# Performance work log

Hardware: AMD Instinct MI355X
Metric: run time of the kernel (lower is better)

Reference implementation:

```python
import jax, jax.numpy as jnp
import numpy as np

D_MODEL = 1024
N_HEADS = 16
THETA = 10000.0


def _rope(x, token_positions):
    # x: (b, h, s, d_k); token_positions: (b, s)
    d_k = x.shape[-1]
    powers = jnp.arange(0, d_k, 2, dtype=jnp.float32) / d_k        # (d_k/2,)
    freqs = 1.0 / (THETA ** powers)
    ang = token_positions.astype(jnp.float32)[..., None] * freqs   # (b, s, d_k/2)
    cos = jnp.cos(ang)[:, None, :, :].astype(x.dtype)              # (b, 1, s, d_k/2)
    sin = jnp.sin(ang)[:, None, :, :].astype(x.dtype)
    x_even = x[..., ::2]
    x_odd = x[..., 1::2]
    r1 = x_even * cos - x_odd * sin
    r2 = x_even * sin + x_odd * cos
    # interleave back to (..., d_k)
    return jnp.stack([r1, r2], axis=-1).reshape(x.shape)


def reference(x, token_positions, wq, wk, wv, wo):
    B, S, D = x.shape
    H = N_HEADS
    d_k = D // H

    def proj(w):
        y = jnp.einsum('bsi,oi->bso', x, w)
        return y.reshape(B, S, H, d_k).transpose(0, 2, 1, 3)  # (b, h, s, d_k)

    q = _rope(proj(wq), token_positions)
    k = _rope(proj(wk), token_positions)
    v = proj(wv)

    scale = 1.0 / jnp.sqrt(jnp.asarray(d_k, dtype=x.dtype))
    score = jnp.einsum('bhqd,bhkd->bhqk', q, k) * scale  # (b, h, s, s)
    causal = jnp.tril(jnp.ones((S, S), dtype=bool))
    score = jnp.where(causal, score, -jnp.inf)
    probs = jax.nn.softmax(score, axis=-1)
    attn = jnp.einsum('bhqk,bhkd->bhqd', probs, v)
    attn = attn.transpose(0, 2, 1, 3).reshape(B, S, D)
    return jnp.einsum('bsi,oi->bso', attn, wo)


def setup_inputs() -> dict:
    key = jax.random.key(0)
    ks = jax.random.split(key, 6)
    B, S, D = 2, 2048, D_MODEL
    std = (2.0 / (D + D)) ** 0.5
    x = jax.random.normal(ks[0], (B, S, D), dtype=jnp.float32)
    token_positions = jnp.broadcast_to(jnp.arange(S, dtype=jnp.int32), (B, S))
    wq = jax.random.normal(ks[1], (D, D), dtype=jnp.float32) * std
    wk = jax.random.normal(ks[2], (D, D), dtype=jnp.float32) * std
    wv = jax.random.normal(ks[3], (D, D), dtype=jnp.float32) * std
    wo = jax.random.normal(ks[4], (D, D), dtype=jnp.float32) * std
    return {"x": x, "token_positions": token_positions, "wq": wq, "wk": wk, "wv": wv, "wo": wo}
```

## Files before the change

### kernel.cpp

```cpp
#include <hip/hip_runtime.h>
#include <hip/hip_bf16.h>

typedef unsigned short u16;
typedef unsigned int u32;
typedef short short8 __attribute__((ext_vector_type(8)));
typedef u16 u16x8 __attribute__((ext_vector_type(8)));
typedef u16 u16x4 __attribute__((ext_vector_type(4)));
typedef u32 u32x4 __attribute__((ext_vector_type(4)));
typedef float f32x4 __attribute__((ext_vector_type(4)));
typedef float f32x16 __attribute__((ext_vector_type(16)));

#define MFMA(a, b, c) __builtin_amdgcn_mfma_f32_16x16x32_bf16((a), (b), (c), 0, 0, 0)
#define MFMA32(a, b, c) __builtin_amdgcn_mfma_f32_32x32x16_bf16((a), (b), (c), 0, 0, 0)

#define QSCALE 0.18033688011112042f

__device__ __forceinline__ u16 f2bf(float f) {
  unsigned u = __float_as_uint(f);
  unsigned r = (u + 0x7fffu + ((u >> 16) & 1u)) >> 16;
  return (u16)r;
}
__device__ __forceinline__ float bf2f(u16 h) {
  return __uint_as_float(((unsigned)h) << 16);
}
__device__ __forceinline__ float exp2hw(float x) {
  float r;
  asm("v_exp_f32 %0, %1" : "=v"(r) : "v"(x));
  return r;
}
__device__ __forceinline__ u32 cvtpk(float lo, float hi) {
  u32 d;
  asm("v_cvt_pk_bf16_f32 %0, %1, %2" : "=v"(d) : "v"(lo), "v"(hi));
  return d;
}
__device__ __forceinline__ void plswap(u32& a, u32& b) {
  asm volatile("v_permlane32_swap_b32 %0, %1" : "+v"(a), "+v"(b));
}
__device__ __forceinline__ void async16(const void* g, void* l) {
  __builtin_amdgcn_global_load_lds(
      (const __attribute__((address_space(1))) void*)g,
      (__attribute__((address_space(3))) void*)l, 16, 0, 0);
}
__device__ __forceinline__ f32x16 zero16() {
  f32x16 z;
#pragma unroll
  for (int i = 0; i < 16; i++) z[i] = 0.f;
  return z;
}
#define WAITV(N) asm volatile("s_waitcnt vmcnt(" #N ")" ::: "memory")
#define WAITL0() asm volatile("s_waitcnt lgkmcnt(0)" ::: "memory")
#define BAR() __builtin_amdgcn_s_barrier()
#define PRIO1 __builtin_amdgcn_s_setprio(1)
#define PRIO0 __builtin_amdgcn_s_setprio(0)

__global__ __launch_bounds__(256) void convert_kernel(
    const float* __restrict__ x, const float* __restrict__ wq,
    const float* __restrict__ wk, const float* __restrict__ wv,
    const float* __restrict__ wo, u16* __restrict__ ws) {
  int blk = blockIdx.x;
  const float* src; u16* dst;
  if (blk < 2048)      { src = x;  dst = ws; }
  else if (blk < 2560) { src = wq; dst = ws + 4194304;               blk -= 2048; }
  else if (blk < 3072) { src = wk; dst = ws + 4194304 + 1048576;     blk -= 2560; }
  else if (blk < 3584) { src = wv; dst = ws + 4194304 + 2 * 1048576; blk -= 3072; }
  else                 { src = wo; dst = ws + 4194304 + 3 * 1048576; blk -= 3584; }
  int idx = (blk * 256 + threadIdx.x) * 8;
  float4 v0 = *(const float4*)(src + idx);
  float4 v1 = *(const float4*)(src + idx + 4);
  u16x8 o;
  o[0] = f2bf(v0.x); o[1] = f2bf(v0.y); o[2] = f2bf(v0.z); o[3] = f2bf(v0.w);
  o[4] = f2bf(v1.x); o[5] = f2bf(v1.y); o[6] = f2bf(v1.z); o[7] = f2bf(v1.w);
  *(u16x8*)(dst + idx) = o;
}

__global__ __launch_bounds__(256) void rope_table(const int* __restrict__ tp,
                                                  float* __restrict__ tab) {
  int t = blockIdx.x * 256 + threadIdx.x;
  int bs = t >> 5, p = t & 31;
  float freq = exp2hw(-(float)p * 0.4152410118609203f);
  float ang = (float)tp[bs] * freq;
  float sn, cs;
  sincosf(ang, &sn, &cs);
  tab[bs * 64 + p * 2] = cs;
  tab[bs * 64 + p * 2 + 1] = sn;
}

__global__ __launch_bounds__(512, 2) void gemm_qkv256(
    const u16* __restrict__ xb, const u16* __restrict__ Wg,
    const float* __restrict__ tab, u16* __restrict__ qb, u16* __restrict__ kb,
    u16* __restrict__ vt) {
  __shared__ u16 As[2][16384];
  __shared__ u16 Bs[2][12288];
  const int tid = threadIdx.x, lane = tid & 63, wid = tid >> 6;
  const int wm = wid >> 2, wn = wid & 3;
  const int g = lane >> 4, r = lane & 15;
  const int rowBase = blockIdx.y << 8;
  const int colBase = blockIdx.x * 192;

#define STG_A(BUF, T)                                                         \
  do {                                                                        \
    _Pragma("unroll") for (int i_ = 0; i_ < 4; ++i_) {                        \
      int c = i_ * 512 + tid;                                                 \
      int row = c >> 3, kc = ((c & 7) ^ (row & 7)) * 8;                       \
      async16(xb + (size_t)(rowBase + row) * 1024 + (T)*64 + kc,              \
              (char*)As[BUF] + c * 16);                                       \
    }                                                                         \
  } while (0)
#define STG_B(BUF, T)                                                         \
  do {                                                                        \
    _Pragma("unroll") for (int i_ = 0; i_ < 3; ++i_) {                        \
      int c = i_ * 512 + tid;                                                 \
      int row = c >> 3, kc = ((c & 7) ^ (row & 7)) * 8;                       \
      async16(Wg + (size_t)(colBase + row) * 1024 + (T)*64 + kc,              \
              (char*)Bs[BUF] + c * 16);                                       \
    }                                                                         \
  } while (0)

  f32x4 acc[8][3];
#pragma unroll
  for (int m = 0; m < 8; m++)
#pragma unroll
    for (int n = 0; n < 3; n++) acc[m][n] = (f32x4){0.f, 0.f, 0.f, 0.f};
  short8 af[4][2], bfr[3][2];

#define RD_A(CUR, MH)                                                         \
  do {                                                                        \
    _Pragma("unroll") for (int mi = 0; mi < 4; mi++) {                        \
      int ra = wm * 128 + (MH)*64 + mi * 16 + r;                              \
      const u16* p = As[CUR] + ra * 64;                                       \
      int sw = (ra & 7) << 3;                                                 \
      af[mi][0] = *(const short8*)(p + ((g << 3) ^ sw));                      \
      af[mi][1] = *(const short8*)(p + (((4 + g) << 3) ^ sw));                \
    }                                                                         \
  } while (0)
#define RD_B(CUR)                                                             \
  do {                                                                        \
    _Pragma("unroll") for (int ni = 0; ni < 3; ni++) {                        \
      int cb = wn * 48 + ni * 16 + r;                                         \
      const u16* p = Bs[CUR] + cb * 64;                                       \
      int sw = (cb & 7) << 3;                                                 \
      bfr[ni][0] = *(const short8*)(p + ((g << 3) ^ sw));                     \
      bfr[ni][1] = *(const short8*)(p + (((4 + g) << 3) ^ sw));               \
    }                                                                         \
  } while (0)
#define MM24(MH)                                                              \
  do {                                                                        \
    _Pragma("unroll") for (int mi = 0; mi < 4; mi++)                          \
        _Pragma("unroll") for (int ni = 0; ni < 3; ni++) {                    \
      acc[(MH)*4 + mi][ni] = MFMA(af[mi][0], bfr[ni][0], acc[(MH)*4 + mi][ni]); \
      acc[(MH)*4 + mi][ni] = MFMA(af[mi][1], bfr[ni][1], acc[(MH)*4 + mi][ni]); \
    }                                                                         \
  } while (0)

  STG_A(0, 0); STG_B(0, 0);
  STG_A(1, 1);
  WAITV(4);
  BAR();

  for (int t = 0; t < 16; ++t) {
    const int cur = t & 1, nxt = cur ^ 1;
    RD_A(cur, 0);
    RD_B(cur);
    if (t < 15) STG_B(nxt, t + 1);
    BAR(); WAITL0();
    PRIO1; MM24(0); PRIO0; BAR();
    RD_A(cur, 1);
    if (t < 14) {
      STG_A(cur, t + 2);
      WAITV(4);
    } else {
      WAITV(0);
    }
    BAR(); WAITL0();
    PRIO1; MM24(1); PRIO0; BAR();
  }
#undef STG_A
#undef STG_B
#undef RD_A
#undef RD_B
#undef MM24

  const int colF = colBase + wn * 48;
#pragma unroll
  for (int n = 0; n < 3; n++) {
    const int col3 = colF + n * 16 + r;
    const int z = col3 >> 10;
    const int col = col3 & 1023;
    if (z < 2) {
      u16* dst = z ? kb : qb;
      const float qs = z ? 1.0f : QSCALE;
      const int p2 = (col >> 1) & 31;
      const bool odd = col & 1;
#pragma unroll
      for (int m = 0; m < 8; m++)
#pragma unroll
        for (int i = 0; i < 4; i++) {
          const int row = rowBase + wm * 128 + m * 16 + g * 4 + i;
          float2 cssn = *(const float2*)(tab + row * 64 + p2 * 2);
          float v = acc[m][n][i];
          float part = __shfl_xor(v, 1);
          float res = odd ? (part * cssn.y + v * cssn.x)
                          : (v * cssn.x - part * cssn.y);
          dst[(size_t)row * 1024 + col] = f2bf(res * qs);
        }
    } else {
#pragma unroll
      for (int m = 0; m < 8; m++)
#pragma unroll
        for (int i = 0; i < 4; i++) {
          const int row = rowBase + wm * 128 + m * 16 + g * 4 + i;
          const int bb = row >> 11, s = row & 2047;
          vt[(size_t)((bb * 16 + (col >> 6)) * 64 + (col & 63)) * 2048 + s] =
              f2bf(acc[m][n][i]);
        }
    }
  }
}

__device__ __forceinline__ void gemm_tile(const u16* __restrict__ A,
                                          const u16* __restrict__ Bm, int K,
                                          int rowBase, int colBase, u16* As,
                                          u16* Bs, f32x4 acc[4][4]) {
  const int tid = threadIdx.x;
  const int lane = tid & 63, wid = tid >> 6;
  const int wr = wid >> 1, wc = wid & 1;
  const int g = lane >> 4, r = lane & 15;

#pragma unroll
  for (int m = 0; m < 4; m++)
#pragma unroll
    for (int n = 0; n < 4; n++) acc[m][n] = (f32x4){0.f, 0.f, 0.f, 0.f};

#define GSTAGE(KT, BUF)                                                       \
  do {                                                                        \
    _Pragma("unroll") for (int i_ = 0; i_ < 4; ++i_) {                        \
      int c = i_ * 256 + tid;                                                 \
      int row = c >> 3, kc = (c & 7) ^ (row & 7);                             \
      async16(A + (size_t)(rowBase + row) * K + ((KT) << 6) + kc * 8,         \
              (char*)As + (BUF)*16384 + c * 16);                              \
    }                                                                         \
    _Pragma("unroll") for (int i_ = 0; i_ < 4; ++i_) {                        \
      int c = i_ * 256 + tid;                                                 \
      int row = c >> 3, kc = (c & 7) ^ (row & 7);                             \
      async16(Bm + (size_t)(colBase + row) * K + ((KT) << 6) + kc * 8,        \
              (char*)Bs + (BUF)*16384 + c * 16);                              \
    }                                                                         \
  } while (0)

  const int nkt = K >> 6;
  GSTAGE(0, 0);
  for (int kt = 0; kt < nkt; ++kt) {
    const int cur = kt & 1;
    if (kt + 1 < nkt) {
      GSTAGE(kt + 1, cur ^ 1);
      WAITV(8);
    } else {
      WAITV(0);
    }
    BAR();
    const u16* Ab = As + cur * 8192;
    const u16* Bb = Bs + cur * 8192;
#pragma unroll
    for (int ks = 0; ks < 2; ++ks) {
      short8 af[4], bfr[4];
#pragma unroll
      for (int m = 0; m < 4; m++) {
        int rr = wr * 64 + m * 16 + r;
        af[m] = *(const short8*)(Ab + rr * 64 + (((ks * 4 + g) ^ (rr & 7)) << 3));
      }
#pragma unroll
      for (int n = 0; n < 4; n++) {
        int rr = wc * 64 + n * 16 + r;
        bfr[n] = *(const short8*)(Bb + rr * 64 + (((ks * 4 + g) ^ (rr & 7)) << 3));
      }
#pragma unroll
      for (int m = 0; m < 4; m++)
#pragma unroll
        for (int n = 0; n < 4; n++)
          acc[m][n] = MFMA(af[m], bfr[n], acc[m][n]);
    }
    WAITL0();
    BAR();
  }
#undef GSTAGE
}

__global__ __launch_bounds__(256, 4) void attn_kernel(
    const u16* __restrict__ qg, const u16* __restrict__ kg,
    const u16* __restrict__ vt, u16* __restrict__ p0, u16* __restrict__ p1,
    float* __restrict__ mbuf, float* __restrict__ lbuf) {
  __shared__ u16 Ks[2][64 * 64];
  __shared__ u16 Vs[2][64 * 64];
  const int tid = threadIdx.x, wid = tid >> 6, lane = tid & 63;
  const int q5 = lane & 31, hi = lane >> 5;
  const int akc = blockIdx.x >> 5, bh = blockIdx.x & 31;
  const int a = akc >> 2, k = (akc >> 1) & 1, c = akc & 1;
  const int b = bh >> 4, h = bh & 15;
  const int base = (wid < 2) ? a : (15 - a);
  const int rb = base * 128 + k * 64 + (wid & 1) * 32;
  const int cmax = rb >> 5;
  const int jend = 30 - 2 * a + k;
  const int qrow = (b << 11) + rb + q5;

  short8 bq[4];
  {
    const u16* qp = qg + (size_t)qrow * 1024 + (h << 6) + hi * 8;
    bq[0] = *(const short8*)(qp);
    bq[1] = *(const short8*)(qp + 16);
    bq[2] = *(const short8*)(qp + 32);
    bq[3] = *(const short8*)(qp + 48);
  }
  f32x16 accO0 = zero16(), accO1 = zero16();
  float m_r = -1e30f, l_r = 0.f;

#define STAGE(JT, BUF)                                                        \
  do {                                                                        \
    _Pragma("unroll") for (int i_ = 0; i_ < 2; i_++) {                        \
      int cc_ = i_ * 256 + tid;                                               \
      int row = cc_ >> 3, cc = (cc_ & 7) ^ (row & 7);                         \
      async16(kg + (size_t)((b << 11) + ((JT) << 6) + row) * 1024 +           \
                  (h << 6) + cc * 8,                                          \
              (char*)Ks[BUF] + cc_ * 16);                                     \
      async16(vt + (size_t)((bh << 6) + row) * 2048 + ((JT) << 6) + cc * 8,   \
              (char*)Vs[BUF] + cc_ * 16);                                     \
    }                                                                         \
  } while (0)

  if (c <= jend) STAGE(c, 0);

  for (int jj = c; jj <= jend; jj += 2) {
    const int cur = ((jj - c) >> 1) & 1;
    if (jj + 2 <= jend) {
      STAGE(jj + 2, cur ^ 1);
      WAITV(4);
    } else {
      WAITV(0);
    }
    BAR();
    if (2 * jj <= cmax) {
      const u16* Kb = Ks[cur];
      const u16* Vb = Vs[cur];
      const bool has1 = (2 * jj + 1 <= cmax);
      const int rsw = (q5 & 7) << 3;
      f32x16 s0 = zero16(), s1 = zero16();
      PRIO1;
#pragma unroll
      for (int kk = 0; kk < 4; kk++) {
        short8 kf =
            *(const short8*)(Kb + q5 * 64 + ((((kk << 1) + hi) << 3) ^ rsw));
        s0 = MFMA32(kf, bq[kk], s0);
      }
      PRIO0;
      if (has1) {
        PRIO1;
#pragma unroll
        for (int kk = 0; kk < 4; kk++) {
          short8 kf = *(const short8*)(Kb + (32 + q5) * 64 +
                                       ((((kk << 1) + hi) << 3) ^ rsw));
          s1 = MFMA32(kf, bq[kk], s1);
        }
        PRIO0;
      }
      if (2 * jj == cmax) {
#pragma unroll
        for (int rg = 0; rg < 16; rg++) {
          int rowk = (rg & 3) + 8 * (rg >> 2) + 4 * hi;
          if (rowk > q5) s0[rg] = -1e30f;
        }
      } else if (2 * jj + 1 == cmax) {
#pragma unroll
        for (int rg = 0; rg < 16; rg++) {
          int rowk = (rg & 3) + 8 * (rg >> 2) + 4 * hi;
          if (rowk > q5) s1[rg] = -1e30f;
        }
      }
      float pmax = s0[0];
#pragma unroll
      for (int rg = 1; rg < 16; rg++) pmax = fmaxf(pmax, s0[rg]);
      if (has1) {
#pragma unroll
        for (int rg = 0; rg < 16; rg++) pmax = fmaxf(pmax, s1[rg]);
      }
      pmax = fmaxf(pmax, __shfl_xor(pmax, 32));
      if (!__all(pmax <= m_r + 8.0f)) {
        float mn = fmaxf(m_r, pmax);
        float sc = exp2hw(m_r - mn);
        l_r *= sc;
#pragma unroll
        for (int rg = 0; rg < 16; rg++) {
          accO0[rg] *= sc;
          accO1[rg] *= sc;
        }
        m_r = mn;
      }
      float rs = 0.f;
      u32 pw00[4], pw01[4], pw10[4], pw11[4];
#define PACK(SREG, OUT, S16)                                                  \
  do {                                                                        \
    float pp0 = exp2hw(SREG[(S16)*8 + 0] - m_r);                              \
    float pp1 = exp2hw(SREG[(S16)*8 + 1] - m_r);                              \
    float pp2 = exp2hw(SREG[(S16)*8 + 2] - m_r);                              \
    float pp3 = exp2hw(SREG[(S16)*8 + 3] - m_r);                              \
    float pp4 = exp2hw(SREG[(S16)*8 + 4] - m_r);                              \
    float pp5 = exp2hw(SREG[(S16)*8 + 5] - m_r);                              \
    float pp6 = exp2hw(SREG[(S16)*8 + 6] - m_r);                              \
    float pp7 = exp2hw(SREG[(S16)*8 + 7] - m_r);                              \
    rs += ((pp0 + pp1) + (pp2 + pp3)) + ((pp4 + pp5) + (pp6 + pp7));          \
    u32 X = cvtpk(pp0, pp1), Y = cvtpk(pp2, pp3);                             \
    u32 U = cvtpk(pp4, pp5), W = cvtpk(pp6, pp7);                             \
    plswap(X, U);                                                             \
    plswap(Y, W);                                                             \
    OUT[0] = X; OUT[1] = Y; OUT[2] = U; OUT[3] = W;                           \
  } while (0)
      PACK(s0, pw00, 0);
      PACK(s0, pw01, 1);
      if (has1) {
        PACK(s1, pw10, 0);
        PACK(s1, pw11, 1);
      }
#undef PACK
      rs += __shfl_xor(rs, 32);
      l_r += rs;
#define PVSTEP(PW, CH)                                                        \
  do {                                                                        \
    u32x4 pv_ = {PW[0], PW[1], PW[2], PW[3]};                                 \
    short8 pb_ = __builtin_bit_cast(short8, pv_);                             \
    short8 v0_ =                                                              \
        *(const short8*)(Vb + q5 * 64 + ((((CH) + hi) << 3) ^ rsw));          \
    short8 v1_ = *(const short8*)(Vb + (32 + q5) * 64 +                       \
                                  ((((CH) + hi) << 3) ^ rsw));                \
    accO0 = MFMA32(v0_, pb_, accO0);                                          \
    accO1 = MFMA32(v1_, pb_, accO1);                                          \
  } while (0)
      PRIO1;
      PVSTEP(pw00, 0);
      PVSTEP(pw01, 2);
      if (has1) {
        PVSTEP(pw10, 4);
        PVSTEP(pw11, 6);
      }
      PRIO0;
#undef PVSTEP
    }
    WAITL0();
    BAR();
  }
#undef STAGE

  u16* pout = c ? p1 : p0;
#pragma unroll
  for (int qd = 0; qd < 4; qd++) {
    u16x4 o0, o1;
#pragma unroll
    for (int e = 0; e < 4; e++) {
      o0[e] = f2bf(accO0[qd * 4 + e]);
      o1[e] = f2bf(accO1[qd * 4 + e]);
    }
    u16* op = pout + (size_t)qrow * 1024 + (h << 6) + qd * 8 + hi * 4;
    *(u16x4*)(op) = o0;
    *(u16x4*)(op + 32) = o1;
  }
  if (hi == 0) {
    int mli = c * 65536 + (bh << 11) + rb + q5;
    mbuf[mli] = m_r;
    lbuf[mli] = l_r;
  }
}

__global__ __launch_bounds__(256) void attn_merge(const u16* __restrict__ p1,
                                                  const float* __restrict__ mbuf,
                                                  const float* __restrict__ lbuf,
                                                  u16* __restrict__ ab) {
  int t = blockIdx.x * 256 + threadIdx.x;
  int dg = t & 7, row = t >> 3;
  int bh = row >> 11, s = row & 2047;
  int b = bh >> 4, h = bh & 15;
  size_t addr = (size_t)((b << 11) + s) * 1024 + (h << 6) + dg * 8;
  float m0 = mbuf[row], m1 = mbuf[65536 + row];
  float l0 = lbuf[row], l1 = lbuf[65536 + row];
  float m = fmaxf(m0, m1);
  float w0 = exp2hw(m0 - m), w1 = exp2hw(m1 - m);
  float inv = 1.0f / (l0 * w0 + l1 * w1);
  u16x8 o0 = *(const u16x8*)(ab + addr);
  u16x8 o1 = *(const u16x8*)(p1 + addr);
  u16x8 o;
#pragma unroll
  for (int i = 0; i < 8; i++)
    o[i] = f2bf((bf2f(o0[i]) * w0 + bf2f(o1[i]) * w1) * inv);
  *(u16x8*)(ab + addr) = o;
}

__global__ __launch_bounds__(256) void gemm_ao(const u16* __restrict__ ab,
                                               const u16* __restrict__ wob,
                                               float* __restrict__ out) {
  __shared__ u16 As[2][128 * 64], Bs[2][128 * 64];
  f32x4 acc[4][4];
  gemm_tile(ab, wob, 1024, blockIdx.y * 128, blockIdx.x * 128, As[0], Bs[0], acc);
  const int lane = threadIdx.x & 63, wid = threadIdx.x >> 6;
  const int wr = wid >> 1, wc = wid & 1, g = lane >> 4, r = lane & 15;
  const int rowB = blockIdx.y * 128 + wr * 64;
  const int colB = blockIdx.x * 128 + wc * 64;
#pragma unroll
  for (int m = 0; m < 4; m++)
#pragma unroll
    for (int n = 0; n < 4; n++)
#pragma unroll
      for (int i = 0; i < 4; i++)
        out[(size_t)(rowB + m * 16 + g * 4 + i) * 1024 + colB + n * 16 + r] =
            acc[m][n][i];
}

extern "C" void kernel_launch(void* const* d_in, const int* in_sizes, int n_in,
                              void* d_out, int out_size, void* d_ws,
                              size_t ws_size, hipStream_t stream) {
  const float* x = (const float*)d_in[0];
  const int* tp = (const int*)d_in[1];
  const float* wq = (const float*)d_in[2];
  const float* wk = (const float*)d_in[3];
  const float* wv = (const float*)d_in[4];
  const float* wo = (const float*)d_in[5];
  float* out = (float*)d_out;

  u16* ws = (u16*)d_ws;
  u16* xb = ws;
  u16* wqb = xb + 4194304;
  u16* wkb = wqb + 1048576;
  u16* wvb = wkb + 1048576;
  u16* wob = wvb + 1048576;
  u16* qb = wob + 1048576;
  u16* kb = qb + 4194304;
  u16* vtb = kb + 4194304;
  u16* ab = vtb + 4194304;
  float* tab = (float*)ab;
  float* mbuf = (float*)wqb;
  float* lbuf = (float*)wkb;

  convert_kernel<<<4096, 256, 0, stream>>>(x, wq, wk, wv, wo, ws);
  rope_table<<<512, 256, 0, stream>>>(tp, tab);
  gemm_qkv256<<<dim3(16, 16), 512, 0, stream>>>(xb, wqb, tab, qb, kb, vtb);
  attn_kernel<<<1024, 256, 0, stream>>>(qb, kb, vtb, ab, xb, mbuf, lbuf);
  attn_merge<<<2048, 256, 0, stream>>>(xb, mbuf, lbuf, ab);
  gemm_ao<<<dim3(8, 32), 256, 0, stream>>>(ab, wob, out);
}
```

Measured before the change: 115.5 us.

## Split attention KV range four ways with single-buffer LDS and fuse rope table

Attention now splits each query block's key range into four interleaved chunks instead of two, doubling the grid to 2048 blocks. It drops LDS double buffering to single buffers and raises the launch-bounds occupancy target from 4 to 7. The merge kernel combines four partials, and the rope table generation is folded into the convert kernel to save a launch. The intent is more parallelism and occupancy, at the cost of losing load/compute overlap within a block, extra partial-output traffic, and more merge work.

```diff
diff --git a/kernel.cpp b/kernel.cpp
--- a/kernel.cpp
+++ b/kernel.cpp
@@ -56,8 +56,20 @@
 __global__ __launch_bounds__(256) void convert_kernel(
     const float* __restrict__ x, const float* __restrict__ wq,
     const float* __restrict__ wk, const float* __restrict__ wv,
-    const float* __restrict__ wo, u16* __restrict__ ws) {
+    const float* __restrict__ wo, u16* __restrict__ ws,
+    const int* __restrict__ tp, float* __restrict__ tab) {
   int blk = blockIdx.x;
+  if (blk >= 4096) {
+    int t = (blk - 4096) * 256 + threadIdx.x;
+    int bs = t >> 5, p = t & 31;
+    float freq = exp2hw(-(float)p * 0.4152410118609203f);
+    float ang = (float)tp[bs] * freq;
+    float sn, cs;
+    sincosf(ang, &sn, &cs);
+    tab[bs * 64 + p * 2] = cs;
+    tab[bs * 64 + p * 2 + 1] = sn;
+    return;
+  }
   const float* src; u16* dst;
   if (blk < 2048)      { src = x;  dst = ws; }
   else if (blk < 2560) { src = wq; dst = ws + 4194304;               blk -= 2048; }
@@ -71,18 +83,6 @@
   o[0] = f2bf(v0.x); o[1] = f2bf(v0.y); o[2] = f2bf(v0.z); o[3] = f2bf(v0.w);
   o[4] = f2bf(v1.x); o[5] = f2bf(v1.y); o[6] = f2bf(v1.z); o[7] = f2bf(v1.w);
   *(u16x8*)(dst + idx) = o;
-}
-
-__global__ __launch_bounds__(256) void rope_table(const int* __restrict__ tp,
-                                                  float* __restrict__ tab) {
-  int t = blockIdx.x * 256 + threadIdx.x;
-  int bs = t >> 5, p = t & 31;
-  float freq = exp2hw(-(float)p * 0.4152410118609203f);
-  float ang = (float)tp[bs] * freq;
-  float sn, cs;
-  sincosf(ang, &sn, &cs);
-  tab[bs * 64 + p * 2] = cs;
-  tab[bs * 64 + p * 2 + 1] = sn;
 }
 
 __global__ __launch_bounds__(512, 2) void gemm_qkv256(
@@ -285,16 +285,17 @@
 #undef GSTAGE
 }
 
-__global__ __launch_bounds__(256, 4) void attn_kernel(
+__global__ __launch_bounds__(256, 7) void attn_kernel(
     const u16* __restrict__ qg, const u16* __restrict__ kg,
     const u16* __restrict__ vt, u16* __restrict__ p0, u16* __restrict__ p1,
-    float* __restrict__ mbuf, float* __restrict__ lbuf) {
-  __shared__ u16 Ks[2][64 * 64];
-  __shared__ u16 Vs[2][64 * 64];
+    u16* __restrict__ p2, u16* __restrict__ p3, float* __restrict__ mbuf,
+    float* __restrict__ lbuf) {
+  __shared__ u16 Ks[64 * 64];
+  __shared__ u16 Vs[64 * 64];
   const int tid = threadIdx.x, wid = tid >> 6, lane = tid & 63;
   const int q5 = lane & 31, hi = lane >> 5;
   const int akc = blockIdx.x >> 5, bh = blockIdx.x & 31;
-  const int a = akc >> 2, k = (akc >> 1) & 1, c = akc & 1;
+  const int a = akc >> 3, k = (akc >> 2) & 1, c = akc & 3;
   const int b = bh >> 4, h = bh & 15;
   const int base = (wid < 2) ? a : (15 - a);
   const int rb = base * 128 + k * 64 + (wid & 1) * 32;
@@ -313,33 +314,25 @@
   f32x16 accO0 = zero16(), accO1 = zero16();
   float m_r = -1e30f, l_r = 0.f;
 
-#define STAGE(JT, BUF)                                                        \
+#define STAGE(JT)                                                             \
   do {                                                                        \
     _Pragma("unroll") for (int i_ = 0; i_ < 2; i_++) {                        \
       int cc_ = i_ * 256 + tid;                                               \
       int row = cc_ >> 3, cc = (cc_ & 7) ^ (row & 7);                         \
       async16(kg + (size_t)((b << 11) + ((JT) << 6) + row) * 1024 +           \
                   (h << 6) + cc * 8,                                          \
-              (char*)Ks[BUF] + cc_ * 16);                                     \
+              (char*)Ks + cc_ * 16);                                          \
       async16(vt + (size_t)((bh << 6) + row) * 2048 + ((JT) << 6) + cc * 8,   \
-              (char*)Vs[BUF] + cc_ * 16);                                     \
-    }                                                                         \
-  } while (0)
-
-  if (c <= jend) STAGE(c, 0);
-
-  for (int jj = c; jj <= jend; jj += 2) {
-    const int cur = ((jj - c) >> 1) & 1;
-    if (jj + 2 <= jend) {
-      STAGE(jj + 2, cur ^ 1);
-      WAITV(4);
-    } else {
-      WAITV(0);
-    }
+              (char*)Vs + cc_ * 16);                                          \
+    }                                                                         \
+  } while (0)
+
+  STAGE(c);
+
+  for (int jj = c; jj <= jend; jj += 4) {
+    WAITV(0);
     BAR();
     if (2 * jj <= cmax) {
-      const u16* Kb = Ks[cur];
-      const u16* Vb = Vs[cur];
       const bool has1 = (2 * jj + 1 <= cmax);
       const int rsw = (q5 & 7) << 3;
       f32x16 s0 = zero16(), s1 = zero16();
@@ -347,7 +340,7 @@
 #pragma unroll
       for (int kk = 0; kk < 4; kk++) {
         short8 kf =
-            *(const short8*)(Kb + q5 * 64 + ((((kk << 1) + hi) << 3) ^ rsw));
+            *(const short8*)(Ks + q5 * 64 + ((((kk << 1) + hi) << 3) ^ rsw));
         s0 = MFMA32(kf, bq[kk], s0);
       }
       PRIO0;
@@ -355,7 +348,7 @@
         PRIO1;
 #pragma unroll
         for (int kk = 0; kk < 4; kk++) {
-          short8 kf = *(const short8*)(Kb + (32 + q5) * 64 +
+          short8 kf = *(const short8*)(Ks + (32 + q5) * 64 +
                                        ((((kk << 1) + hi) << 3) ^ rsw));
           s1 = MFMA32(kf, bq[kk], s1);
         }
@@ -426,8 +419,8 @@
     u32x4 pv_ = {PW[0], PW[1], PW[2], PW[3]};                                 \
     short8 pb_ = __builtin_bit_cast(short8, pv_);                             \
     short8 v0_ =                                                              \
-        *(const short8*)(Vb + q5 * 64 + ((((CH) + hi) << 3) ^ rsw));          \
-    short8 v1_ = *(const short8*)(Vb + (32 + q5) * 64 +                       \
+        *(const short8*)(Vs + q5 * 64 + ((((CH) + hi) << 3) ^ rsw));          \
+    short8 v1_ = *(const short8*)(Vs + (32 + q5) * 64 +                       \
                                   ((((CH) + hi) << 3) ^ rsw));                \
     accO0 = MFMA32(v0_, pb_, accO0);                                          \
     accO1 = MFMA32(v1_, pb_, accO1);                                          \
@@ -444,10 +437,11 @@
     }
     WAITL0();
     BAR();
+    if (jj + 4 <= jend) STAGE(jj + 4);
   }
 #undef STAGE
 
-  u16* pout = c ? p1 : p0;
+  u16* pout = (c == 0) ? p0 : (c == 1) ? p1 : (c == 2) ? p2 : p3;
 #pragma unroll
   for (int qd = 0; qd < 4; qd++) {
     u16x4 o0, o1;
@@ -467,26 +461,33 @@
   }
 }
 
-__global__ __launch_bounds__(256) void attn_merge(const u16* __restrict__ p1,
-                                                  const float* __restrict__ mbuf,
-                                                  const float* __restrict__ lbuf,
-                                                  u16* __restrict__ ab) {
+__global__ __launch_bounds__(256) void attn_merge(
+    const u16* __restrict__ p1, const u16* __restrict__ p2,
+    const u16* __restrict__ p3, const float* __restrict__ mbuf,
+    const float* __restrict__ lbuf, u16* __restrict__ ab) {
   int t = blockIdx.x * 256 + threadIdx.x;
   int dg = t & 7, row = t >> 3;
   int bh = row >> 11, s = row & 2047;
   int b = bh >> 4, h = bh & 15;
   size_t addr = (size_t)((b << 11) + s) * 1024 + (h << 6) + dg * 8;
   float m0 = mbuf[row], m1 = mbuf[65536 + row];
+  float m2 = mbuf[131072 + row], m3 = mbuf[196608 + row];
   float l0 = lbuf[row], l1 = lbuf[65536 + row];
-  float m = fmaxf(m0, m1);
+  float l2 = lbuf[131072 + row], l3 = lbuf[196608 + row];
+  float m = fmaxf(fmaxf(m0, m1), fmaxf(m2, m3));
   float w0 = exp2hw(m0 - m), w1 = exp2hw(m1 - m);
-  float inv = 1.0f / (l0 * w0 + l1 * w1);
+  float w2 = exp2hw(m2 - m), w3 = exp2hw(m3 - m);
+  float inv = 1.0f / (l0 * w0 + l1 * w1 + l2 * w2 + l3 * w3);
   u16x8 o0 = *(const u16x8*)(ab + addr);
   u16x8 o1 = *(const u16x8*)(p1 + addr);
+  u16x8 o2 = *(const u16x8*)(p2 + addr);
+  u16x8 o3 = *(const u16x8*)(p3 + addr);
   u16x8 o;
 #pragma unroll
   for (int i = 0; i < 8; i++)
-    o[i] = f2bf((bf2f(o0[i]) * w0 + bf2f(o1[i]) * w1) * inv);
+    o[i] = f2bf((bf2f(o0[i]) * w0 + bf2f(o1[i]) * w1 + bf2f(o2[i]) * w2 +
+                 bf2f(o3[i]) * w3) *
+                inv);
   *(u16x8*)(ab + addr) = o;
 }
 
@@ -531,14 +532,16 @@
   u16* kb = qb + 4194304;
   u16* vtb = kb + 4194304;
   u16* ab = vtb + 4194304;
+  u16* pt2 = ab + 4194304;
+  u16* pt3 = pt2 + 4194304;
   float* tab = (float*)ab;
   float* mbuf = (float*)wqb;
-  float* lbuf = (float*)wkb;
-
-  convert_kernel<<<4096, 256, 0, stream>>>(x, wq, wk, wv, wo, ws);
-  rope_table<<<512, 256, 0, stream>>>(tp, tab);
+  float* lbuf = (float*)wvb;
+
+  convert_kernel<<<4608, 256, 0, stream>>>(x, wq, wk, wv, wo, ws, tp, tab);
   gemm_qkv256<<<dim3(16, 16), 512, 0, stream>>>(xb, wqb, tab, qb, kb, vtb);
-  attn_kernel<<<1024, 256, 0, stream>>>(qb, kb, vtb, ab, xb, mbuf, lbuf);
-  attn_merge<<<2048, 256, 0, stream>>>(xb, mbuf, lbuf, ab);
+  attn_kernel<<<2048, 256, 0, stream>>>(qb, kb, vtb, ab, xb, pt2, pt3, mbuf,
+                                        lbuf);
+  attn_merge<<<2048, 256, 0, stream>>>(xb, pt2, pt3, mbuf, lbuf, ab);
   gemm_ao<<<dim3(8, 32), 256, 0, stream>>>(ab, wob, out);
 }
```

After: 273.8 us. +137.1%, slower.
